# Kernel tuning notes

Measured on AMD Instinct MI355X. Metric: run time of the kernel, lower is better.

The kernel has to match this reference:

```python
import jax, jax.numpy as jnp
import numpy as np

S, B, D, F = 2048, 8, 1024, 4096
EPS = 1e-5

def setup_inputs() -> dict:
    key = jax.random.key(0)
    ks = jax.random.split(key, 16)
    sc = lambda fan_in: 1.0 / np.sqrt(fan_in)
    inp = {
        'src': jax.random.normal(ks[0], (S, B, D), dtype=jnp.float32),
        'wq': jax.random.uniform(ks[1], (D, D), jnp.float32, -sc(D), sc(D)),
        'bq': jnp.zeros((D,), jnp.float32),
        'wk': jax.random.uniform(ks[2], (D, D), jnp.float32, -sc(D), sc(D)),
        'bk': jnp.zeros((D,), jnp.float32),
        'wv': jax.random.uniform(ks[3], (D, D), jnp.float32, -sc(D), sc(D)),
        'bv': jnp.zeros((D,), jnp.float32),
        'wo': jax.random.uniform(ks[4], (D, D), jnp.float32, -sc(D), sc(D)),
        'bo': jnp.zeros((D,), jnp.float32),
        'w1': jax.random.uniform(ks[5], (F, D), jnp.float32, -sc(D), sc(D)),
        'b1': jnp.zeros((F,), jnp.float32),
        'w2': jax.random.uniform(ks[6], (D, F), jnp.float32, -sc(F), sc(F)),
        'b2': jnp.zeros((D,), jnp.float32),
        'g1': jnp.ones((D,), jnp.float32),
        'be1': jnp.zeros((D,), jnp.float32),
        'g2': jnp.ones((D,), jnp.float32),
        'be2': jnp.zeros((D,), jnp.float32),
    }
    return inp

def _layer_norm(x, g, b):
    mu = jnp.mean(x, axis=-1, keepdims=True)
    var = jnp.mean(jnp.square(x - mu), axis=-1, keepdims=True)
    return (x - mu) / jnp.sqrt(var + EPS) * g + b

def _forward(src, wq, bq, wk, bk, wv, bv, wo, bo, w1, b1, w2, b2, g1, be1, g2, be2):
    # Linear attention (ELU+1 feature map, no normalizer — faithful to source)
    Q = jax.nn.elu(src @ wq.T + bq) + 1.0  # [S,B,D]
    K = jax.nn.elu(src @ wk.T + bk) + 1.0  # [S,B,D]
    V = src @ wv.T + bv                    # [S,B,D]
    KV = jnp.einsum('sbd,sbe->bde', K, V)  # [B,D,D]
    attn = jnp.einsum('sbd,bde->sbe', Q, KV)  # [S,B,D]
    attn = attn @ wo.T + bo
    x = _layer_norm(src + attn, g1, be1)   # dropout is identity (p=0 / eval)
    ffn = jax.nn.relu(x @ w1.T + b1) @ w2.T + b2
    return _layer_norm(x + ffn, g2, be2)

def reference(src, wq, bq, wk, bk, wv, bv, wo, bo, w1, b1, w2, b2, g1, be1, g2, be2):
    return _forward(src, wq, bq, wk, bk, wv, bv, wo, bo, w1, b1, w2, b2, g1, be1, g2, be2)
```

## Files before the change

kernel.cpp:

```cpp
#include <hip/hip_runtime.h>
#include <hip/hip_bf16.h>
#include <math.h>


typedef __attribute__((ext_vector_type(8))) short short8;
typedef __attribute__((ext_vector_type(4))) short short4_t;
typedef __attribute__((ext_vector_type(4))) float f32x4;

#define S_DIM 2048
#define B_DIM 8
#define D_DIM 1024
#define F_DIM 4096

__device__ __forceinline__ unsigned short f2bf(float f) {
  __hip_bfloat16 h = __float2bfloat16(f);
  return *reinterpret_cast<unsigned short*>(&h);
}

#define GLD16(gp, sp)                                              \
  __builtin_amdgcn_global_load_lds(                                \
      (const __attribute__((address_space(1))) void*)(gp),         \
      (__attribute__((address_space(3))) void*)(sp), 16, 0, 0)

#define BAR()                                  \
  do {                                         \
    asm volatile("" ::: "memory");             \
    __builtin_amdgcn_s_barrier();              \
    asm volatile("" ::: "memory");             \
  } while (0)
#define WAITVM6() asm volatile("s_waitcnt vmcnt(6)" ::: "memory")
#define WAITVM10() asm volatile("s_waitcnt vmcnt(10)" ::: "memory")
#define WAITVM0() asm volatile("s_waitcnt vmcnt(0)" ::: "memory")
#define SCHED_FENCE() __builtin_amdgcn_sched_barrier(0)

template <int EPI>
__global__ __launch_bounds__(512, 2) void gemm256_kernel(
    const unsigned short* __restrict__ A, long lda, long sA,
    const unsigned short* __restrict__ B, long ldb, long sB,
    void* __restrict__ Cv, long ldc, long sC,
    const float* __restrict__ bias,
    const float* __restrict__ resid, long ldr, long sR, int K) {
  __shared__ short lds[65536];
  const int gx = gridDim.x;
  const int nwg = gx * gridDim.y;
  const int orig = blockIdx.y * gx + blockIdx.x;
  const int cpx = nwg >> 3;
  const int wgid = (orig & 7) * cpx + (orig >> 3);
  const int bx = wgid % gx, by = wgid / gx;
  const int bz = blockIdx.z;
  const unsigned short* Ablk = A + (long)bz * sA + (long)by * 256 * lda;
  const unsigned short* Bblk = B + (long)bz * sB + (long)bx * 256 * ldb;

  const int tid = threadIdx.x;
  const int w = tid >> 6, lane = tid & 63;
  const int wm = w >> 2, wn = w & 3;
  const int lr = lane & 15, kh = lane >> 4;

  const int sr = w * 8 + (lane >> 3);
  const int sc = ((lane & 7) ^ (lane >> 3)) * 8;
  const long aoff0 = (long)sr * lda + sc;
  const long aoff1 = (long)(128 + sr) * lda + sc;
  const int br0 = sr + ((sr >> 5) << 5);
  const int br1 = (64 + sr) + (((64 + sr) >> 5) << 5);
  const long boff0 = (long)br0 * ldb + sc;
  const long boff1 = (long)br1 * ldb + sc;
  const int dst0 = w * 1024;
  const int dst1 = (8 + w) * 1024;

#define STAGE_A(bufOff, h, kt)                                                \
  do {                                                                        \
    const unsigned short* _g = Ablk + (long)(h) * 64 * lda + (long)(kt) * 64; \
    GLD16(_g + aoff0, (char*)lds + (bufOff) + (h)*16384 + dst0);              \
    GLD16(_g + aoff1, (char*)lds + (bufOff) + (h)*16384 + dst1);              \
  } while (0)
#define STAGE_B(bufOff, nh, kt)                                               \
  do {                                                                        \
    const unsigned short* _g = Bblk + (long)(nh) * 32 * ldb + (long)(kt) * 64;\
    GLD16(_g + boff0, (char*)lds + (bufOff) + 32768 + (nh)*16384 + dst0);     \
    GLD16(_g + boff1, (char*)lds + (bufOff) + 32768 + (nh)*16384 + dst1);     \
  } while (0)

  const int chk0 = ((kh ^ (lr & 7)) << 4);
  const int chk1 = (((4 + kh) ^ (lr & 7)) << 4);
  const int aRdBase = (wm * 64 + lr) * 128;
  const int bRdBase = (wn * 32 + lr) * 128;

  short8 af[4][2], b0r[2][2], b1r[2][2];
  f32x4 acc[8][4];
#pragma unroll
  for (int m = 0; m < 8; ++m)
#pragma unroll
    for (int n = 0; n < 4; ++n)
#pragma unroll
      for (int j = 0; j < 4; ++j) acc[m][n][j] = 0.f;

#define LDA_H(bufOff, h)                                                     \
  do {                                                                       \
    const char* _p = (const char*)lds + (bufOff) + (h)*16384 + aRdBase;      \
    _Pragma("unroll") for (int m = 0; m < 4; ++m) {                          \
      af[m][0] = *(const short8*)(_p + m * 2048 + chk0);                     \
      af[m][1] = *(const short8*)(_p + m * 2048 + chk1);                     \
    }                                                                        \
  } while (0)
#define LDB_H(dst, bufOff, nh)                                               \
  do {                                                                       \
    const char* _p = (const char*)lds + (bufOff) + 32768 + (nh)*16384 + bRdBase; \
    _Pragma("unroll") for (int n = 0; n < 2; ++n) {                          \
      dst[n][0] = *(const short8*)(_p + n * 2048 + chk0);                    \
      dst[n][1] = *(const short8*)(_p + n * 2048 + chk1);                    \
    }                                                                        \
  } while (0)
#define MFMA_Q(mh, nh, bset)                                                 \
  do {                                                                       \
    SCHED_FENCE();                                                           \
    __builtin_amdgcn_s_setprio(1);                                           \
    _Pragma("unroll") for (int m = 0; m < 4; ++m)                            \
    _Pragma("unroll") for (int n = 0; n < 2; ++n)                            \
    _Pragma("unroll") for (int ks = 0; ks < 2; ++ks)                         \
      acc[(mh)*4 + m][(nh)*2 + n] = __builtin_amdgcn_mfma_f32_16x16x32_bf16( \
          af[m][ks], bset[n][ks], acc[(mh)*4 + m][(nh)*2 + n], 0, 0, 0);     \
    __builtin_amdgcn_s_setprio(0);                                           \
    SCHED_FENCE();                                                           \
  } while (0)

  const int T = K >> 6;
  STAGE_A(0, 0, 0); STAGE_B(0, 0, 0); STAGE_B(0, 1, 0); STAGE_A(0, 1, 0);
  STAGE_A(65536, 0, 1); STAGE_B(65536, 0, 1); STAGE_B(65536, 1, 1);
  WAITVM10(); BAR();
  LDB_H(b0r, 0, 0);

  for (int i = 0; i < (T >> 1); ++i) {
    const int kto  = 2 * i + 1;
    const int kte2 = (2 * i + 2 < T) ? (2 * i + 2) : (T - 1);
    const int kto2 = (2 * i + 3 < T) ? (2 * i + 3) : (T - 1);
    LDA_H(0, 0); STAGE_A(65536, 1, kto);
    BAR(); MFMA_Q(0, 0, b0r); BAR();
    LDB_H(b1r, 0, 1); STAGE_A(0, 0, kte2);
    BAR(); MFMA_Q(0, 1, b1r); BAR();
    LDA_H(0, 1); STAGE_B(0, 0, kte2);
    BAR(); MFMA_Q(1, 1, b1r); BAR();
    STAGE_B(0, 1, kte2);
    WAITVM6(); BAR(); MFMA_Q(1, 0, b0r); LDB_H(b0r, 65536, 0); BAR();
    LDA_H(65536, 0); STAGE_A(0, 1, kte2);
    BAR(); MFMA_Q(0, 0, b0r); BAR();
    LDB_H(b1r, 65536, 1); STAGE_A(65536, 0, kto2);
    BAR(); MFMA_Q(0, 1, b1r); BAR();
    LDA_H(65536, 1); STAGE_B(65536, 0, kto2);
    BAR(); MFMA_Q(1, 1, b1r); BAR();
    STAGE_B(65536, 1, kto2);
    WAITVM6(); BAR(); MFMA_Q(1, 0, b0r); LDB_H(b0r, 0, 0); BAR();
  }
  WAITVM0();

  const long gm0 = (long)by * 256 + wm * 128;
  const long gn0 = (long)bx * 256 + wn * 64;
  if constexpr (EPI == 4) {
    float* C = (float*)Cv + (long)bz * sC;
    const float* R = resid + (long)bz * sR;
#pragma unroll
    for (int mg = 0; mg < 8; ++mg)
#pragma unroll
      for (int ng = 0; ng < 4; ++ng) {
        const long col = gn0 + ng * 16 + lr;
        const float bcol = bias[col];
#pragma unroll
        for (int j = 0; j < 4; ++j) {
          const long row = gm0 + mg * 16 + kh * 4 + j;
          C[row * ldc + col] = acc[mg][ng][j] + bcol + R[row * ldr + col];
        }
      }
  } else {
    unsigned short* C = (unsigned short*)Cv + (long)bz * sC;
    const bool do_elu = (EPI == 5) && (gn0 < 2048);
#pragma unroll
    for (int mg = 0; mg < 8; ++mg)
#pragma unroll
      for (int ng = 0; ng < 4; ++ng) {
        const long col = gn0 + ng * 16 + lr;
        const float bcol = bias[col];
#pragma unroll
        for (int j = 0; j < 4; ++j) {
          const long row = gm0 + mg * 16 + kh * 4 + j;
          float v = acc[mg][ng][j] + bcol;
          if constexpr (EPI == 3) v = fmaxf(v, 0.f);
          if constexpr (EPI == 5) {
            if (do_elu) v = (v > 0.f) ? (v + 1.f) : expf(v);
          }
          C[row * ldc + col] = f2bf(v);
        }
      }
  }
#undef STAGE_A
#undef STAGE_B
#undef LDA_H
#undef LDB_H
#undef MFMA_Q
}

template <int EPI>
__global__ __launch_bounds__(256, 2) void gemm_bt_kernel(
    const unsigned short* __restrict__ A, long lda, long sA,
    const unsigned short* __restrict__ B, long ldb, long sB,
    void* __restrict__ Cv, long ldc, long sC,
    const float* __restrict__ bias,
    const float* __restrict__ resid, long ldr, long sR, int K) {
  __shared__ short As[128 * 32];
  __shared__ short Bs[128 * 32];
  const int gx = gridDim.x;
  const int nwg = gx * gridDim.y;
  const int orig = blockIdx.y * gx + blockIdx.x;
  const int cpx = nwg >> 3;
  const int wgid = (orig & 7) * cpx + (orig >> 3);
  const int bx = wgid % gx;
  const int by = wgid / gx;

  const int bz = blockIdx.z;
  const unsigned short* Ab = A + (long)bz * sA + (long)by * 128 * lda;
  const unsigned short* Bb = B + (long)bz * sB + (long)bx * 128 * ldb;
  const int tid = threadIdx.x;
  const int w = tid >> 6, lane = tid & 63;
  const int srow = lane >> 2;
  const int scol = (lane & 3) * 8;
  const int wr = (w >> 1) * 64, wc = (w & 1) * 64;
  const int lr = lane & 15, kh = lane >> 4;

  f32x4 acc[4][4];
#pragma unroll
  for (int m = 0; m < 4; ++m)
#pragma unroll
    for (int n = 0; n < 4; ++n)
#pragma unroll
      for (int j = 0; j < 4; ++j) acc[m][n][j] = 0.f;

  const unsigned short* ga0 = Ab + (long)(w * 16 + srow) * lda + scol;
  const unsigned short* ga1 = Ab + (long)(64 + w * 16 + srow) * lda + scol;
  const unsigned short* gb0 = Bb + (long)(w * 16 + srow) * ldb + scol;
  const unsigned short* gb1 = Bb + (long)(64 + w * 16 + srow) * ldb + scol;
  short* la0 = &As[(w * 16) * 32];
  short* la1 = &As[(64 + w * 16) * 32];
  short* lb0 = &Bs[(w * 16) * 32];
  short* lb1 = &Bs[(64 + w * 16) * 32];

  for (int k0 = 0; k0 < K; k0 += 32) {
    GLD16(ga0 + k0, la0);
    GLD16(ga1 + k0, la1);
    GLD16(gb0 + k0, lb0);
    GLD16(gb1 + k0, lb1);
    __syncthreads();
    short8 af[4], bf[4];
#pragma unroll
    for (int m = 0; m < 4; ++m)
      af[m] = *(const short8*)&As[(wr + m * 16 + lr) * 32 + kh * 8];
#pragma unroll
    for (int n = 0; n < 4; ++n)
      bf[n] = *(const short8*)&Bs[(wc + n * 16 + lr) * 32 + kh * 8];
#pragma unroll
    for (int m = 0; m < 4; ++m)
#pragma unroll
      for (int n = 0; n < 4; ++n)
        acc[m][n] =
            __builtin_amdgcn_mfma_f32_16x16x32_bf16(af[m], bf[n], acc[m][n], 0, 0, 0);
    __syncthreads();
  }

  const long gm0 = (long)by * 128 + wr;
  const long gn0 = (long)bx * 128 + wc;
  unsigned short* C = (unsigned short*)Cv + (long)bz * sC;
#pragma unroll
  for (int m = 0; m < 4; ++m)
#pragma unroll
    for (int n = 0; n < 4; ++n) {
      const long col = gn0 + n * 16 + lr;
#pragma unroll
      for (int j = 0; j < 4; ++j) {
        const long row = gm0 + m * 16 + kh * 4 + j;
        C[row * ldc + col] = f2bf(acc[m][n][j]);
      }
    }
}

__global__ __launch_bounds__(256) void transpose_kernel(
    const unsigned short* __restrict__ in, unsigned short* __restrict__ out,
    long ld) {
  __shared__ unsigned short t[64][68];
  const int b = blockIdx.z;
  const long s0 = (long)blockIdx.x * 64, d0 = (long)blockIdx.y * 64;
  const int tid = threadIdx.x;
  {
    const int r = tid >> 3, c = (tid & 7) * 8;
#pragma unroll
    for (int it = 0; it < 2; ++it) {
      const int s = r + it * 32;
      const unsigned short* g = &in[((s0 + s) * B_DIM + b) * ld + d0 + c];
      short4_t v0 = *(const short4_t*)g;
      short4_t v1 = *(const short4_t*)(g + 4);
      *(short4_t*)&t[s][c] = v0;
      *(short4_t*)&t[s][c + 4] = v1;
    }
  }
  __syncthreads();
  {
    const int d = tid >> 3, c = (tid & 7) * 8;
#pragma unroll
    for (int it = 0; it < 2; ++it) {
      const int dd = d + it * 32;
      short8 v;
#pragma unroll
      for (int j = 0; j < 8; ++j) v[j] = (short)t[c + j][dd];
      *(short8*)&out[(long)b * ((long)D_DIM * S_DIM) + (d0 + dd) * S_DIM + s0 + c] = v;
    }
  }
}

template <int WRITE_BF16>
__global__ __launch_bounds__(256) void layernorm_kernel(
    const float* in, float* outf, unsigned short* __restrict__ outb,
    const float* __restrict__ gamma, const float* __restrict__ beta) {
  const long row = blockIdx.x;
  const float* x = in + row * D_DIM;
  const int tid = threadIdx.x;
  const int lane = tid & 63, w = tid >> 6;
  f32x4 v = *(const f32x4*)&x[tid * 4];
  float s = v[0] + v[1] + v[2] + v[3];
  float q = v[0] * v[0] + v[1] * v[1] + v[2] * v[2] + v[3] * v[3];
#pragma unroll
  for (int off = 32; off > 0; off >>= 1) {
    s += __shfl_down(s, off, 64);
    q += __shfl_down(q, off, 64);
  }
  __shared__ float red[8];
  if (lane == 0) { red[w] = s; red[w + 4] = q; }
  __syncthreads();
  s = red[0] + red[1] + red[2] + red[3];
  q = red[4] + red[5] + red[6] + red[7];
  const float mu = s * (1.f / D_DIM);
  const float var = q * (1.f / D_DIM) - mu * mu;
  const float rs = rsqrtf(var + 1e-5f);
  f32x4 g = *(const f32x4*)&gamma[tid * 4];
  f32x4 bb = *(const f32x4*)&beta[tid * 4];
  f32x4 o;
#pragma unroll
  for (int j = 0; j < 4; ++j) o[j] = (v[j] - mu) * rs * g[j] + bb[j];
  *(f32x4*)&outf[row * D_DIM + tid * 4] = o;
  if constexpr (WRITE_BF16) {
    short4_t ob;
#pragma unroll
    for (int j = 0; j < 4; ++j) ob[j] = (short)f2bf(o[j]);
    *(short4_t*)&outb[row * D_DIM + tid * 4] = ob;
  }
}

__global__ __launch_bounds__(256) void cast_kernel(
    const float* __restrict__ in, unsigned short* __restrict__ out, long n) {
  long i = ((long)blockIdx.x * 256 + threadIdx.x) * 8;
  if (i >= n) return;
  f32x4 a = *(const f32x4*)&in[i];
  f32x4 b = *(const f32x4*)&in[i + 4];
  short8 v;
#pragma unroll
  for (int j = 0; j < 4; ++j) v[j] = (short)f2bf(a[j]);
#pragma unroll
  for (int j = 0; j < 4; ++j) v[4 + j] = (short)f2bf(b[j]);
  *(short8*)&out[i] = v;
}

extern "C" void kernel_launch(void* const* d_in, const int* in_sizes, int n_in,
                              void* d_out, int out_size, void* d_ws, size_t ws_size,
                              hipStream_t stream) {
  const float* src = (const float*)d_in[0];
  const float* wq  = (const float*)d_in[1];
  const float* bq  = (const float*)d_in[2];
  const float* wk  = (const float*)d_in[3];
  const float* bk  = (const float*)d_in[4];
  const float* wv  = (const float*)d_in[5];
  const float* bv  = (const float*)d_in[6];
  const float* wo  = (const float*)d_in[7];
  const float* bo  = (const float*)d_in[8];
  const float* w1  = (const float*)d_in[9];
  const float* b1  = (const float*)d_in[10];
  const float* w2  = (const float*)d_in[11];
  const float* b2  = (const float*)d_in[12];
  const float* g1  = (const float*)d_in[13];
  const float* be1 = (const float*)d_in[14];
  const float* g2  = (const float*)d_in[15];
  const float* be2 = (const float*)d_in[16];

  const long MB = 1024L * 1024L;
  if (ws_size < 248 * MB) return;
  char* ws = (char*)d_ws;
  unsigned short* w1b   = (unsigned short*)(ws + 0 * MB);
  unsigned short* w2b   = (unsigned short*)(ws + 8 * MB);
  unsigned short* srcb  = (unsigned short*)(ws + 16 * MB);
  unsigned short* Kt    = (unsigned short*)(ws + 16 * MB);
  unsigned short* Vt    = (unsigned short*)(ws + 48 * MB);
  float*          AO    = (float*)(ws + 16 * MB);
  float*          X     = (float*)(ws + 16 * MB);
  unsigned short* KVm   = (unsigned short*)(ws + 80 * MB);
  unsigned short* Mt    = (unsigned short*)(ws + 96 * MB);
  unsigned short* Xb    = (unsigned short*)(ws + 80 * MB);
  unsigned short* wqkvb = (unsigned short*)(ws + 112 * MB);
  float*          bqkv  = (float*)(ws + 118 * MB);
  unsigned short* wob   = (unsigned short*)(ws + 119 * MB);
  unsigned short* QKVb  = (unsigned short*)(ws + 144 * MB);
  unsigned short* H     = (unsigned short*)(ws + 112 * MB);

  const dim3 blk(256);
  const dim3 blk512(512);
  cast_kernel<<<dim3(512), blk, 0, stream>>>(wq, wqkvb, 1048576);
  cast_kernel<<<dim3(512), blk, 0, stream>>>(wk, wqkvb + 1048576, 1048576);
  cast_kernel<<<dim3(512), blk, 0, stream>>>(wv, wqkvb + 2097152, 1048576);
  cast_kernel<<<dim3(512), blk, 0, stream>>>(wo, wob, 1048576);
  cast_kernel<<<dim3(2048), blk, 0, stream>>>(w1, w1b, 4194304);
  cast_kernel<<<dim3(2048), blk, 0, stream>>>(w2, w2b, 4194304);
  cast_kernel<<<dim3(8192), blk, 0, stream>>>(src, srcb, 16777216);
  hipMemcpyAsync(bqkv, bq, 4096, hipMemcpyDeviceToDevice, stream);
  hipMemcpyAsync(bqkv + 1024, bk, 4096, hipMemcpyDeviceToDevice, stream);
  hipMemcpyAsync(bqkv + 2048, bv, 4096, hipMemcpyDeviceToDevice, stream);

  gemm256_kernel<5><<<dim3(12, 64, 1), blk512, 0, stream>>>(
      srcb, 1024, 0, wqkvb, 1024, 0, QKVb, 3072, 0, bqkv, nullptr, 0, 0, 1024);

  transpose_kernel<<<dim3(32, 16, 8), blk, 0, stream>>>(QKVb + 1024, Kt, 3072);
  transpose_kernel<<<dim3(32, 16, 8), blk, 0, stream>>>(QKVb + 2048, Vt, 3072);

  gemm_bt_kernel<0><<<dim3(8, 8, 8), blk, 0, stream>>>(
      Kt, 2048, 2097152, Vt, 2048, 2097152, KVm, 1024, 1048576,
      nullptr, nullptr, 0, 0, 2048);
  gemm_bt_kernel<0><<<dim3(8, 8, 8), blk, 0, stream>>>(
      wob, 1024, 0, KVm, 1024, 1048576, Mt, 1024, 1048576,
      nullptr, nullptr, 0, 0, 1024);
  gemm256_kernel<4><<<dim3(4, 8, 8), blk512, 0, stream>>>(
      QKVb, 24576, 3072, Mt, 1024, 1048576, AO, 8192, 1024,
      bo, src, 8192, 1024, 1024);

  layernorm_kernel<1><<<dim3(16384), blk, 0, stream>>>(AO, X, Xb, g1, be1);

  gemm256_kernel<3><<<dim3(16, 64, 1), blk512, 0, stream>>>(
      Xb, 1024, 0, w1b, 1024, 0, H, 4096, 0, b1, nullptr, 0, 0, 1024);
  gemm256_kernel<4><<<dim3(4, 64, 1), blk512, 0, stream>>>(
      H, 4096, 0, w2b, 4096, 0, (float*)d_out, 1024, 0,
      b2, X, 1024, 0, 4096);

  layernorm_kernel<0><<<dim3(16384), blk, 0, stream>>>(
      (float*)d_out, (float*)d_out, nullptr, g2, be2);
}
```

Baseline: 647.5 us.

## Peel last GEMM iteration, use incremental pointers and explicit LDS waits

Restructures the GEMM main loop: global load addresses become running pointers advanced each iteration instead of being recomputed from the k-tile index, and the final double iteration is peeled so the tail issues no redundant clamped loads. Scheduler fences around MFMA blocks are replaced with an explicit lgkmcnt(0) wait followed by a sched barrier before each MFMA group. This aims to cut address arithmetic and wasted loads at the tail, at the risk of changing the compiler's instruction interleaving. The last MFMA in the loop body keeps its LDS reads unfenced, which is a hazard if the compiler does not insert the needed waits itself.

```diff
diff --git a/kernel.cpp b/kernel.cpp
--- a/kernel.cpp
+++ b/kernel.cpp
@@ -31,7 +31,11 @@
 #define WAITVM6() asm volatile("s_waitcnt vmcnt(6)" ::: "memory")
 #define WAITVM10() asm volatile("s_waitcnt vmcnt(10)" ::: "memory")
 #define WAITVM0() asm volatile("s_waitcnt vmcnt(0)" ::: "memory")
-#define SCHED_FENCE() __builtin_amdgcn_sched_barrier(0)
+#define LGKM0_FENCE()                                        \
+  do {                                                       \
+    asm volatile("s_waitcnt lgkmcnt(0)" ::: "memory");       \
+    __builtin_amdgcn_sched_barrier(0);                       \
+  } while (0)
 
 template <int EPI>
 __global__ __launch_bounds__(512, 2) void gemm256_kernel(
@@ -58,26 +62,27 @@
 
   const int sr = w * 8 + (lane >> 3);
   const int sc = ((lane & 7) ^ (lane >> 3)) * 8;
-  const long aoff0 = (long)sr * lda + sc;
-  const long aoff1 = (long)(128 + sr) * lda + sc;
   const int br0 = sr + ((sr >> 5) << 5);
-  const int br1 = (64 + sr) + (((64 + sr) >> 5) << 5);
-  const long boff0 = (long)br0 * ldb + sc;
-  const long boff1 = (long)br1 * ldb + sc;
+  const unsigned short* pA = Ablk + (long)sr * lda + sc;
+  const unsigned short* pB = Bblk + (long)br0 * ldb + sc;
+  const long dA1 = 128 * lda, dAh = 64 * lda;
+  const long dB1 = 128 * ldb, dBh = 32 * ldb;
   const int dst0 = w * 1024;
   const int dst1 = (8 + w) * 1024;
 
-#define STAGE_A(bufOff, h, kt)                                                \
+#define STAGE_A(bufOff, h, rel)                                               \
   do {                                                                        \
-    const unsigned short* _g = Ablk + (long)(h) * 64 * lda + (long)(kt) * 64; \
-    GLD16(_g + aoff0, (char*)lds + (bufOff) + (h)*16384 + dst0);              \
-    GLD16(_g + aoff1, (char*)lds + (bufOff) + (h)*16384 + dst1);              \
-  } while (0)
-#define STAGE_B(bufOff, nh, kt)                                               \
+    GLD16(pA + (h) * dAh + (rel) * 64,                                        \
+          (char*)lds + (bufOff) + (h)*16384 + dst0);                          \
+    GLD16(pA + (h) * dAh + dA1 + (rel) * 64,                                  \
+          (char*)lds + (bufOff) + (h)*16384 + dst1);                          \
+  } while (0)
+#define STAGE_B(bufOff, nh, rel)                                              \
   do {                                                                        \
-    const unsigned short* _g = Bblk + (long)(nh) * 32 * ldb + (long)(kt) * 64;\
-    GLD16(_g + boff0, (char*)lds + (bufOff) + 32768 + (nh)*16384 + dst0);     \
-    GLD16(_g + boff1, (char*)lds + (bufOff) + 32768 + (nh)*16384 + dst1);     \
+    GLD16(pB + (nh) * dBh + (rel) * 64,                                       \
+          (char*)lds + (bufOff) + 32768 + (nh)*16384 + dst0);                 \
+    GLD16(pB + (nh) * dBh + dB1 + (rel) * 64,                                 \
+          (char*)lds + (bufOff) + 32768 + (nh)*16384 + dst1);                 \
   } while (0)
 
   const int chk0 = ((kh ^ (lr & 7)) << 4);
@@ -112,7 +117,6 @@
   } while (0)
 #define MFMA_Q(mh, nh, bset)                                                 \
   do {                                                                       \
-    SCHED_FENCE();                                                           \
     __builtin_amdgcn_s_setprio(1);                                           \
     _Pragma("unroll") for (int m = 0; m < 4; ++m)                            \
     _Pragma("unroll") for (int n = 0; n < 2; ++n)                            \
@@ -120,7 +124,6 @@
       acc[(mh)*4 + m][(nh)*2 + n] = __builtin_amdgcn_mfma_f32_16x16x32_bf16( \
           af[m][ks], bset[n][ks], acc[(mh)*4 + m][(nh)*2 + n], 0, 0, 0);     \
     __builtin_amdgcn_s_setprio(0);                                           \
-    SCHED_FENCE();                                                           \
   } while (0)
 
   const int T = K >> 6;
@@ -129,28 +132,40 @@
   WAITVM10(); BAR();
   LDB_H(b0r, 0, 0);
 
-  for (int i = 0; i < (T >> 1); ++i) {
-    const int kto  = 2 * i + 1;
-    const int kte2 = (2 * i + 2 < T) ? (2 * i + 2) : (T - 1);
-    const int kto2 = (2 * i + 3 < T) ? (2 * i + 3) : (T - 1);
-    LDA_H(0, 0); STAGE_A(65536, 1, kto);
-    BAR(); MFMA_Q(0, 0, b0r); BAR();
-    LDB_H(b1r, 0, 1); STAGE_A(0, 0, kte2);
-    BAR(); MFMA_Q(0, 1, b1r); BAR();
-    LDA_H(0, 1); STAGE_B(0, 0, kte2);
-    BAR(); MFMA_Q(1, 1, b1r); BAR();
-    STAGE_B(0, 1, kte2);
+  for (int i = 0; i < (T >> 1) - 1; ++i) {
+    LDA_H(0, 0); STAGE_A(65536, 1, 1);
+    BAR(); LGKM0_FENCE(); MFMA_Q(0, 0, b0r); BAR();
+    LDB_H(b1r, 0, 1); STAGE_A(0, 0, 2);
+    BAR(); LGKM0_FENCE(); MFMA_Q(0, 1, b1r); BAR();
+    LDA_H(0, 1); STAGE_B(0, 0, 2);
+    BAR(); LGKM0_FENCE(); MFMA_Q(1, 1, b1r); BAR();
+    STAGE_B(0, 1, 2);
     WAITVM6(); BAR(); MFMA_Q(1, 0, b0r); LDB_H(b0r, 65536, 0); BAR();
-    LDA_H(65536, 0); STAGE_A(0, 1, kte2);
-    BAR(); MFMA_Q(0, 0, b0r); BAR();
-    LDB_H(b1r, 65536, 1); STAGE_A(65536, 0, kto2);
-    BAR(); MFMA_Q(0, 1, b1r); BAR();
-    LDA_H(65536, 1); STAGE_B(65536, 0, kto2);
-    BAR(); MFMA_Q(1, 1, b1r); BAR();
-    STAGE_B(65536, 1, kto2);
+    LDA_H(65536, 0); STAGE_A(0, 1, 2);
+    BAR(); LGKM0_FENCE(); MFMA_Q(0, 0, b0r); BAR();
+    LDB_H(b1r, 65536, 1); STAGE_A(65536, 0, 3);
+    BAR(); LGKM0_FENCE(); MFMA_Q(0, 1, b1r); BAR();
+    LDA_H(65536, 1); STAGE_B(65536, 0, 3);
+    BAR(); LGKM0_FENCE(); MFMA_Q(1, 1, b1r); BAR();
+    STAGE_B(65536, 1, 3);
     WAITVM6(); BAR(); MFMA_Q(1, 0, b0r); LDB_H(b0r, 0, 0); BAR();
-  }
-  WAITVM0();
+    pA += 128; pB += 128;
+  }
+
+  LDA_H(0, 0); STAGE_A(65536, 1, 1);
+  BAR(); LGKM0_FENCE(); MFMA_Q(0, 0, b0r); BAR();
+  LDB_H(b1r, 0, 1);
+  BAR(); LGKM0_FENCE(); MFMA_Q(0, 1, b1r); BAR();
+  LDA_H(0, 1);
+  BAR(); LGKM0_FENCE(); MFMA_Q(1, 1, b1r); BAR();
+  WAITVM0(); BAR(); MFMA_Q(1, 0, b0r); LDB_H(b0r, 65536, 0); BAR();
+  LDA_H(65536, 0);
+  BAR(); LGKM0_FENCE(); MFMA_Q(0, 0, b0r); BAR();
+  LDB_H(b1r, 65536, 1);
+  BAR(); LGKM0_FENCE(); MFMA_Q(0, 1, b1r); BAR();
+  LDA_H(65536, 1);
+  BAR(); LGKM0_FENCE(); MFMA_Q(1, 1, b1r); BAR();
+  LGKM0_FENCE(); MFMA_Q(1, 0, b0r);
 
   const long gm0 = (long)by * 256 + wm * 128;
   const long gn0 = (long)bx * 256 + wn * 64;
```

Result: no change. 650.6 us (+0.5%).
